# Performance work log

Measured on AMD Instinct MI355X. Metric: run time of the kernel, lower is better.

Reference implementation:

```python
import jax, jax.numpy as jnp
import numpy as np


def setup_inputs() -> dict:
    key = jax.random.key(0)
    ks = jax.random.split(key, 8)
    B, C, H, W = 8, 256, 64, 64
    r = 32  # channels // reduction
    return {
        "x": jax.random.normal(ks[0], (B, C, H, W), dtype=jnp.float32),
        "wq": jax.random.normal(ks[1], (r, C), dtype=jnp.float32) * 0.02,
        "bq": jax.random.normal(ks[2], (r,), dtype=jnp.float32) * 0.02,
        "wk": jax.random.normal(ks[3], (r, C), dtype=jnp.float32) * 0.02,
        "bk": jax.random.normal(ks[4], (r,), dtype=jnp.float32) * 0.02,
        "wv": jax.random.normal(ks[5], (C, C), dtype=jnp.float32) * 0.02,
        "bv": jax.random.normal(ks[6], (C,), dtype=jnp.float32) * 0.02,
        "gamma": jax.random.normal(ks[7], (1,), dtype=jnp.float32),
    }


def reference(x, wq, bq, wk, bk, wv, bv, gamma):
    B, C, H, W = x.shape
    N = H * W
    r = wq.shape[0]
    scale = r ** (-0.5)
    xf = x.reshape(B, C, N)  # flatten spatial tokens
    # 1x1 convs == per-pixel linear projections
    q = jnp.einsum("rc,bcn->bnr", wq, xf) + bq  # (B, N, r)
    k = jnp.einsum("rc,bcn->brn", wk, xf) + bk[:, None]  # (B, r, N)
    v = jnp.einsum("dc,bcn->bdn", wv, xf) + bv[:, None]  # (B, C, N)
    attn = jax.nn.softmax(jnp.einsum("bnr,brm->bnm", q, k) * scale, axis=-1)  # (B, N, N)
    # out[b,c,n] = sum_m v[b,c,m] * attn[b,n,m]
    out = jnp.einsum("bdm,bnm->bdn", v, attn).reshape(B, C, H, W)
    return x + gamma[0] * out
```

## Files before the change

kernel.cpp:

```cpp
#include <hip/hip_runtime.h>
#include <hip/hip_bf16.h>


typedef float  f32x4   __attribute__((ext_vector_type(4)));
typedef short  short8  __attribute__((ext_vector_type(8)));
typedef unsigned short ushort4v __attribute__((ext_vector_type(4)));
typedef unsigned short ushort8v __attribute__((ext_vector_type(8)));

__device__ __forceinline__ unsigned short f2bf(float f) {
    __hip_bfloat16 h = __float2bfloat16(f);
    return __builtin_bit_cast(unsigned short, h);
}

__global__ __launch_bounds__(256) void wconv_kernel(
    const float* __restrict__ wq, const float* __restrict__ wk,
    const float* __restrict__ wv, unsigned short* __restrict__ Wall)
{
    int i4 = blockIdx.x * 256 + threadIdx.x;
    int e = i4 * 4;
    const float* src; int off;
    if (e < 8192)       { src = wq; off = e; }
    else if (e < 16384) { src = wk; off = e - 8192; }
    else                { src = wv; off = e - 16384; }
    f32x4 v = *(const f32x4*)(src + off);
    ushort4v u;
#pragma unroll
    for (int j = 0; j < 4; ++j) u[j] = f2bf(v[j]);
    *(ushort4v*)(Wall + e) = u;
}

__global__ __launch_bounds__(256) void xpose_kernel(
    const float* __restrict__ x, unsigned short* __restrict__ xT, int C, int N)
{
    const int t  = threadIdx.x;
    const int n  = blockIdx.x * 256 + t;
    const int c0 = blockIdx.y * 64;
    const int b  = blockIdx.z;
    const float* xb = x + ((size_t)b * C + c0) * N + n;

    unsigned short tmp[64];
#pragma unroll
    for (int i = 0; i < 64; ++i)
        tmp[i] = f2bf(xb[(size_t)i * N]);

    unsigned short* dst = xT + ((size_t)b * N + n) * 256 + c0;
#pragma unroll
    for (int i = 0; i < 8; ++i) {
        ushort8v u;
#pragma unroll
        for (int j = 0; j < 8; ++j) u[j] = tmp[i * 8 + j];
        *(ushort8v*)(dst + i * 8) = u;
    }
}

__global__ __launch_bounds__(256) void projmm_kernel(
    const unsigned short* __restrict__ xT,
    const unsigned short* __restrict__ Wall,
    const float* __restrict__ bq, const float* __restrict__ bk,
    const float* __restrict__ bv,
    unsigned short* __restrict__ qa,
    unsigned short* __restrict__ ka,
    unsigned char* __restrict__ vt8,
    int N, float scale)
{
    __shared__ __align__(16) unsigned short xs[64 * 136];
    __shared__ __align__(16) unsigned short ws[64 * 136];

    const int t  = threadIdx.x;
    const int l  = t & 63;
    const int w  = t >> 6;
    const int qi = l & 15;
    const int g  = l >> 4;
    const int n0 = blockIdx.x * 64;
    const int o0 = blockIdx.y * 64;
    const int b  = blockIdx.z;
    const int tile = n0 >> 6;
    const unsigned short* xTb = xT + (size_t)b * N * 256;

    const f32x4 zero4 = {0.f, 0.f, 0.f, 0.f};
    f32x4 acc[4];
#pragma unroll
    for (int nf = 0; nf < 4; ++nf) acc[nf] = zero4;

    for (int kp = 0; kp < 2; ++kp) {
        if (kp) __syncthreads();
        for (int it = w; it < 34; it += 4) {
            int isw = it >= 17;
            int it2 = isw ? it - 17 : it;
            unsigned short* lbase = (isw ? ws : xs) + it2 * 512;
            int ch  = it2 * 64 + l;
            int row = ch / 17;
            int c16 = ch - row * 17;
            int cc  = c16 > 15 ? 15 : c16;
            const unsigned short* src = isw
                ? (Wall + (size_t)(o0 + row) * 256 + kp * 128 + cc * 8)
                : (xTb + (size_t)(n0 + row) * 256 + kp * 128 + cc * 8);
            __builtin_amdgcn_global_load_lds(
                (const __attribute__((address_space(1))) unsigned int*)src,
                (__attribute__((address_space(3))) unsigned int*)lbase, 16, 0, 0);
        }
        __syncthreads();

#pragma unroll
        for (int ks = 0; ks < 4; ++ks) {
            short8 af;
            {
                const unsigned short* ap = ws + (w * 16 + qi) * 136 + ks * 32 + g * 4;
                ushort4v lo = *(const ushort4v*)ap;
                ushort4v hi = *(const ushort4v*)(ap + 16);
#pragma unroll
                for (int j = 0; j < 4; ++j) { af[j] = (short)lo[j]; af[4 + j] = (short)hi[j]; }
            }
#pragma unroll
            for (int nf = 0; nf < 4; ++nf) {
                short8 bf;
                const unsigned short* bp = xs + (nf * 16 + qi) * 136 + ks * 32 + g * 4;
                ushort4v lo = *(const ushort4v*)bp;
                ushort4v hi = *(const ushort4v*)(bp + 16);
#pragma unroll
                for (int j = 0; j < 4; ++j) { bf[j] = (short)lo[j]; bf[4 + j] = (short)hi[j]; }
                acc[nf] = __builtin_amdgcn_mfma_f32_16x16x32_bf16(af, bf, acc[nf], 0, 0, 0);
            }
        }
    }

    if (o0 == 0) {
        const float* bias = (w < 2) ? bq : bk;
        float sc = (w < 2) ? scale : 1.0f;
        unsigned short* dst = (w < 2) ? qa : ka;
#pragma unroll
        for (int nf = 0; nf < 4; ++nf) {
            ushort4v u;
#pragma unroll
            for (int j = 0; j < 4; ++j) {
                int r = (w & 1) * 16 + g * 4 + j;
                u[j] = f2bf((acc[nf][j] + bias[r]) * sc);
            }
            *(ushort4v*)(dst + ((((size_t)b * 64 + tile) * 4 + nf) * 64 + g * 16 + qi) * 8 + (w & 1) * 4) = u;
        }
    } else {
        unsigned char* vtb = vt8 + ((size_t)b * 64 + tile) * 16384;
#pragma unroll
        for (int nf = 0; nf < 4; ++nf) {
            int m = nf * 16 + qi;
            int G   = ((m & 32) ? 4 : 0) + ((m >> 2) & 3);
            int pos = ((m >> 4) & 1) * 4 + (m & 3);
#pragma unroll
            for (int j = 0; j < 4; ++j) {
                int c = o0 - 64 + w * 16 + g * 4 + j;
                int r = __builtin_amdgcn_cvt_pk_fp8_f32(acc[nf][j] + bv[c], 0.f, 0, false);
                vtb[(size_t)c * 64 + ((G ^ ((c >> 1) & 7)) << 3) + pos] = (unsigned char)(r & 0xFF);
            }
        }
    }
}

__global__ __launch_bounds__(512, 4) void attn_kernel(
    const float* __restrict__ x,
    const unsigned short* __restrict__ qa,
    const unsigned short* __restrict__ ka,
    const unsigned char* __restrict__ vt8,
    const float* __restrict__ gamma,
    float* __restrict__ out, int C, int N)
{
    __shared__ __align__(16) unsigned char vs[2][16384];
    __shared__ float mlb[4][64];

    const int t  = threadIdx.x;
    const int l  = t & 63;
    const int w  = t >> 6;
    const int qi = l & 15;
    const int g  = l >> 4;
    const int qg = w & 3;
    const int kh = w >> 2;
    const int tile_q = blockIdx.x;
    const int b  = blockIdx.y;

    const f32x4 zero4 = {0.f, 0.f, 0.f, 0.f};

    short8 qfrag = *(const short8*)(
        qa + ((((size_t)b * 64 + tile_q) * 4 + qg) * 64 + l) * 8);

    const unsigned short* kab = ka + ((size_t)b * 64) * 2048 + (size_t)kh * 1024 + (size_t)l * 8;
    const unsigned char*  vtb = vt8 + ((size_t)b * 64) * 16384;

    auto stage = [&](int buf, int tl) {
        const unsigned char* src = vtb + (size_t)tl * 16384 + w * 2048 + l * 16;
        unsigned char* dst = &vs[buf][w * 2048 + l * 16];
#pragma unroll
        for (int i = 0; i < 2; ++i)
            __builtin_amdgcn_global_load_lds(
                (const __attribute__((address_space(1))) unsigned int*)(src + i * 1024),
                (__attribute__((address_space(3))) unsigned int*)(dst + i * 1024), 16, 0, 0);
    };

    f32x4 o_[16];
#pragma unroll
    for (int cf = 0; cf < 16; ++cf) o_[cf] = zero4;
    float lsum = 0.f;
    long acur;

    stage(0, 0);
    short8 kcur0 = *(const short8*)(kab);
    short8 kcur1 = *(const short8*)(kab + 512);
    {
        f32x4 s0 = __builtin_amdgcn_mfma_f32_16x16x32_bf16(kcur0, qfrag, zero4, 0, 0, 0);
        f32x4 s1 = __builtin_amdgcn_mfma_f32_16x16x32_bf16(kcur1, qfrag, zero4, 0, 0, 0);
        float p[8];
#pragma unroll
        for (int j = 0; j < 4; ++j) { p[j] = __expf(s0[j]); p[4 + j] = __expf(s1[j]); }
#pragma unroll
        for (int j = 0; j < 8; ++j) lsum += p[j];
        int w0 = __builtin_amdgcn_cvt_pk_fp8_f32(p[0], p[1], 0, false);
        w0 = __builtin_amdgcn_cvt_pk_fp8_f32(p[2], p[3], w0, true);
        int w1 = __builtin_amdgcn_cvt_pk_fp8_f32(p[4], p[5], 0, false);
        w1 = __builtin_amdgcn_cvt_pk_fp8_f32(p[6], p[7], w1, true);
        acur = (long)(((unsigned long long)(unsigned int)w0) | ((unsigned long long)(unsigned int)w1 << 32));
    }
    {
        const unsigned short* kn = kab + 2048;
        kcur0 = *(const short8*)(kn);
        kcur1 = *(const short8*)(kn + 512);
    }
    __syncthreads();

    int buf = 0;
    const int voff = (((kh << 2) | g) ^ ((qi >> 1) & 7)) << 3;
    for (int tl = 0; tl < 64; ++tl) {
        if (tl < 63) stage(buf ^ 1, tl + 1);

        f32x4 s0, s1;
        if (tl < 63) {
            s0 = __builtin_amdgcn_mfma_f32_16x16x32_bf16(kcur0, qfrag, zero4, 0, 0, 0);
            s1 = __builtin_amdgcn_mfma_f32_16x16x32_bf16(kcur1, qfrag, zero4, 0, 0, 0);
        }
        if (tl < 62) {
            const unsigned short* kn = kab + (size_t)(tl + 2) * 2048;
            kcur0 = *(const short8*)(kn);
            kcur1 = *(const short8*)(kn + 512);
        }

        const unsigned char* vrow = &vs[buf][qi * 64 + voff];
#pragma unroll
        for (int cf = 0; cf < 16; ++cf) {
            long v8 = *(const long*)(vrow + cf * 1024);
            o_[cf] = __builtin_amdgcn_mfma_f32_16x16x32_fp8_fp8(acur, v8, o_[cf], 0, 0, 0);
        }

        if (tl < 63) {
            float p[8];
#pragma unroll
            for (int j = 0; j < 4; ++j) { p[j] = __expf(s0[j]); p[4 + j] = __expf(s1[j]); }
#pragma unroll
            for (int j = 0; j < 8; ++j) lsum += p[j];
            int w0 = __builtin_amdgcn_cvt_pk_fp8_f32(p[0], p[1], 0, false);
            w0 = __builtin_amdgcn_cvt_pk_fp8_f32(p[2], p[3], w0, true);
            int w1 = __builtin_amdgcn_cvt_pk_fp8_f32(p[4], p[5], 0, false);
            w1 = __builtin_amdgcn_cvt_pk_fp8_f32(p[6], p[7], w1, true);
            acur = (long)(((unsigned long long)(unsigned int)w0) | ((unsigned long long)(unsigned int)w1 << 32));
        }

        __syncthreads();
        buf ^= 1;
    }

    float l_run = lsum;
    l_run += __shfl_xor(l_run, 16);
    l_run += __shfl_xor(l_run, 32);

    float* cbuf = (float*)vs;
    const int lx = l & 31;
    float* bp = cbuf + ((qg * 64) + l) * 32;
    if (kh == 1) {
        mlb[qg][l] = l_run;
#pragma unroll
        for (int cf = 0; cf < 8; ++cf)
#pragma unroll
            for (int j = 0; j < 4; ++j) bp[(cf * 4 + j) ^ lx] = o_[cf][j];
    }
    __syncthreads();

    float cj[4];
    const float gm = gamma[0];
    const float* xb = x + (size_t)b * C * N;
    float* ob = out + (size_t)b * C * N;
    const int ncol = tile_q * 64 + qg * 16 + g * 4;

    if (kh == 0) {
        float lt = l_run + mlb[qg][l];
        float c0 = gm / lt;
#pragma unroll
        for (int j = 0; j < 4; ++j) cj[j] = __shfl(c0, g * 4 + j);
#pragma unroll
        for (int cf = 0; cf < 8; ++cf) {
            int c = cf * 16 + qi;
            f32x4 xv = *(const f32x4*)(xb + (size_t)c * N + ncol);
            f32x4 ov;
#pragma unroll
            for (int j = 0; j < 4; ++j)
                ov[j] = xv[j] + (o_[cf][j] + bp[(cf * 4 + j) ^ lx]) * cj[j];
            *(f32x4*)(ob + (size_t)c * N + ncol) = ov;
        }
    }
    __syncthreads();

    if (kh == 1) {
#pragma unroll
        for (int cf = 0; cf < 8; ++cf)
#pragma unroll
            for (int j = 0; j < 4; ++j) bp[(cf * 4 + j) ^ lx] = o_[8 + cf][j];
    }
    __syncthreads();

    if (kh == 0) {
#pragma unroll
        for (int cf = 0; cf < 8; ++cf) {
            int c = (8 + cf) * 16 + qi;
            f32x4 xv = *(const f32x4*)(xb + (size_t)c * N + ncol);
            f32x4 ov;
#pragma unroll
            for (int j = 0; j < 4; ++j)
                ov[j] = xv[j] + (o_[8 + cf][j] + bp[(cf * 4 + j) ^ lx]) * cj[j];
            *(f32x4*)(ob + (size_t)c * N + ncol) = ov;
        }
    }
}

extern "C" void kernel_launch(void* const* d_in, const int* in_sizes, int n_in,
                              void* d_out, int out_size, void* d_ws, size_t ws_size,
                              hipStream_t stream) {
    const float* x     = (const float*)d_in[0];
    const float* wq    = (const float*)d_in[1];
    const float* bq    = (const float*)d_in[2];
    const float* wk    = (const float*)d_in[3];
    const float* bk    = (const float*)d_in[4];
    const float* wv    = (const float*)d_in[5];
    const float* bv    = (const float*)d_in[6];
    const float* gamma = (const float*)d_in[7];
    float* out = (float*)d_out;

    const int B = 8, C = 256, N = 4096;
    const float scale = 0.17677669529663687f;

    unsigned short* qa   = (unsigned short*)d_ws;
    unsigned short* ka   = qa + (size_t)B * 64 * 4 * 64 * 8;
    unsigned short* xT   = ka + (size_t)B * 64 * 4 * 64 * 8;
    unsigned short* Wall = xT + (size_t)B * N * 256;
    unsigned char*  vt8  = (unsigned char*)(Wall + 81920);

    wconv_kernel<<<80, 256, 0, stream>>>(wq, wk, wv, Wall);
    xpose_kernel<<<dim3(N / 256, C / 64, B), 256, 0, stream>>>(x, xT, C, N);
    projmm_kernel<<<dim3(N / 64, 5, B), 256, 0, stream>>>(
        xT, Wall, bq, bk, bv, qa, ka, vt8, N, scale);
    attn_kernel<<<dim3(N / 64, B), 512, 0, stream>>>(x, qa, ka, vt8, gamma, out, C, N);
}
```

Before: 110.0 us.

## Process two KV tiles per barrier with four-deep V staging buffer

Grows the LDS V buffer from two to four stages and unrolls the attention loop to handle two key tiles between each __syncthreads, prefetching the next two tiles at the top of each iteration. This halves the number of block-wide barriers and lets more async loads stay in flight. In exchange LDS use doubles to about 64KB per block, which can lower the number of resident blocks per CU and so reduce latency hiding.

After: 113.6 us. 1.03x slower.

```diff
diff --git a/kernel.cpp b/kernel.cpp
--- a/kernel.cpp
+++ b/kernel.cpp
@@ -163,7 +163,7 @@
     const float* __restrict__ gamma,
     float* __restrict__ out, int C, int N)
 {
-    __shared__ __align__(16) unsigned char vs[2][16384];
+    __shared__ __align__(16) unsigned char vs[4][16384];
     __shared__ float mlb[4][64];
 
     const int t  = threadIdx.x;
@@ -200,22 +200,38 @@
     float lsum = 0.f;
     long acur;
 
+    auto packP = [&](const f32x4& s0, const f32x4& s1) -> long {
+        float p[8];
+#pragma unroll
+        for (int j = 0; j < 4; ++j) { p[j] = __expf(s0[j]); p[4 + j] = __expf(s1[j]); }
+#pragma unroll
+        for (int j = 0; j < 8; ++j) lsum += p[j];
+        int w0 = __builtin_amdgcn_cvt_pk_fp8_f32(p[0], p[1], 0, false);
+        w0 = __builtin_amdgcn_cvt_pk_fp8_f32(p[2], p[3], w0, true);
+        int w1 = __builtin_amdgcn_cvt_pk_fp8_f32(p[4], p[5], 0, false);
+        w1 = __builtin_amdgcn_cvt_pk_fp8_f32(p[6], p[7], w1, true);
+        return (long)(((unsigned long long)(unsigned int)w0) |
+                      ((unsigned long long)(unsigned int)w1 << 32));
+    };
+
+    const int voff = (((kh << 2) | g) ^ ((qi >> 1) & 7)) << 3;
+    auto pv = [&](int buf) {
+        const unsigned char* vrow = &vs[buf][qi * 64 + voff];
+#pragma unroll
+        for (int cf = 0; cf < 16; ++cf) {
+            long v8 = *(const long*)(vrow + cf * 1024);
+            o_[cf] = __builtin_amdgcn_mfma_f32_16x16x32_fp8_fp8(acur, v8, o_[cf], 0, 0, 0);
+        }
+    };
+
     stage(0, 0);
+    stage(1, 1);
     short8 kcur0 = *(const short8*)(kab);
     short8 kcur1 = *(const short8*)(kab + 512);
     {
         f32x4 s0 = __builtin_amdgcn_mfma_f32_16x16x32_bf16(kcur0, qfrag, zero4, 0, 0, 0);
         f32x4 s1 = __builtin_amdgcn_mfma_f32_16x16x32_bf16(kcur1, qfrag, zero4, 0, 0, 0);
-        float p[8];
-#pragma unroll
-        for (int j = 0; j < 4; ++j) { p[j] = __expf(s0[j]); p[4 + j] = __expf(s1[j]); }
-#pragma unroll
-        for (int j = 0; j < 8; ++j) lsum += p[j];
-        int w0 = __builtin_amdgcn_cvt_pk_fp8_f32(p[0], p[1], 0, false);
-        w0 = __builtin_amdgcn_cvt_pk_fp8_f32(p[2], p[3], w0, true);
-        int w1 = __builtin_amdgcn_cvt_pk_fp8_f32(p[4], p[5], 0, false);
-        w1 = __builtin_amdgcn_cvt_pk_fp8_f32(p[6], p[7], w1, true);
-        acur = (long)(((unsigned long long)(unsigned int)w0) | ((unsigned long long)(unsigned int)w1 << 32));
+        acur = packP(s0, s1);
     }
     {
         const unsigned short* kn = kab + 2048;
@@ -224,44 +240,36 @@
     }
     __syncthreads();
 
-    int buf = 0;
-    const int voff = (((kh << 2) | g) ^ ((qi >> 1) & 7)) << 3;
-    for (int tl = 0; tl < 64; ++tl) {
-        if (tl < 63) stage(buf ^ 1, tl + 1);
-
-        f32x4 s0, s1;
-        if (tl < 63) {
-            s0 = __builtin_amdgcn_mfma_f32_16x16x32_bf16(kcur0, qfrag, zero4, 0, 0, 0);
-            s1 = __builtin_amdgcn_mfma_f32_16x16x32_bf16(kcur1, qfrag, zero4, 0, 0, 0);
-        }
-        if (tl < 62) {
-            const unsigned short* kn = kab + (size_t)(tl + 2) * 2048;
+    for (int p = 0; p < 32; ++p) {
+        const int t0 = 2 * p;
+        if (p < 31) {
+            stage((t0 + 2) & 3, t0 + 2);
+            stage((t0 + 3) & 3, t0 + 3);
+        }
+
+        f32x4 s0 = __builtin_amdgcn_mfma_f32_16x16x32_bf16(kcur0, qfrag, zero4, 0, 0, 0);
+        f32x4 s1 = __builtin_amdgcn_mfma_f32_16x16x32_bf16(kcur1, qfrag, zero4, 0, 0, 0);
+        if (p < 31) {
+            const unsigned short* kn = kab + (size_t)(t0 + 2) * 2048;
             kcur0 = *(const short8*)(kn);
             kcur1 = *(const short8*)(kn + 512);
         }
-
-        const unsigned char* vrow = &vs[buf][qi * 64 + voff];
-#pragma unroll
-        for (int cf = 0; cf < 16; ++cf) {
-            long v8 = *(const long*)(vrow + cf * 1024);
-            o_[cf] = __builtin_amdgcn_mfma_f32_16x16x32_fp8_fp8(acur, v8, o_[cf], 0, 0, 0);
-        }
-
-        if (tl < 63) {
-            float p[8];
-#pragma unroll
-            for (int j = 0; j < 4; ++j) { p[j] = __expf(s0[j]); p[4 + j] = __expf(s1[j]); }
-#pragma unroll
-            for (int j = 0; j < 8; ++j) lsum += p[j];
-            int w0 = __builtin_amdgcn_cvt_pk_fp8_f32(p[0], p[1], 0, false);
-            w0 = __builtin_amdgcn_cvt_pk_fp8_f32(p[2], p[3], w0, true);
-            int w1 = __builtin_amdgcn_cvt_pk_fp8_f32(p[4], p[5], 0, false);
-            w1 = __builtin_amdgcn_cvt_pk_fp8_f32(p[6], p[7], w1, true);
-            acur = (long)(((unsigned long long)(unsigned int)w0) | ((unsigned long long)(unsigned int)w1 << 32));
-        }
+        pv(t0 & 3);
+        acur = packP(s0, s1);
+
+        f32x4 r0, r1;
+        if (p < 31) {
+            r0 = __builtin_amdgcn_mfma_f32_16x16x32_bf16(kcur0, qfrag, zero4, 0, 0, 0);
+            r1 = __builtin_amdgcn_mfma_f32_16x16x32_bf16(kcur1, qfrag, zero4, 0, 0, 0);
+            const unsigned short* kn = kab + (size_t)(t0 + 3) * 2048;
+            kcur0 = *(const short8*)(kn);
+            kcur1 = *(const short8*)(kn + 512);
+        }
+        pv((t0 + 1) & 3);
+        if (p < 31)
+            acur = packP(r0, r1);
 
         __syncthreads();
-        buf ^= 1;
     }
 
     float l_run = lsum;
```
